# Performance work log

Hardware: AMD Instinct MI355X
Metric: run time of the kernel (lower is better)

## Reference

```python
import jax, jax.numpy as jnp
import numpy as np
from jax import lax

VOCAB = 400000
EMB = 300
HIDDEN = 128
OUT = 3
SEQ = 4096


def setup_inputs() -> dict:
    key = jax.random.key(0)
    ks = jax.random.split(key, 8)
    X = jax.random.randint(ks[0], (SEQ,), 0, VOCAB)
    weights = jax.random.normal(ks[1], (VOCAB, EMB), dtype=jnp.float32) * 0.1
    # nn.RNN params (tanh nonlinearity), uniform(-1/sqrt(H), 1/sqrt(H)) like torch
    s = 1.0 / np.sqrt(HIDDEN)
    W_ih = jax.random.uniform(ks[2], (HIDDEN, EMB), minval=-s, maxval=s, dtype=jnp.float32)
    b_ih = jax.random.uniform(ks[3], (HIDDEN,), minval=-s, maxval=s, dtype=jnp.float32)
    W_hh = jax.random.uniform(ks[4], (HIDDEN, HIDDEN), minval=-s, maxval=s, dtype=jnp.float32)
    b_hh = jax.random.uniform(ks[5], (HIDDEN,), minval=-s, maxval=s, dtype=jnp.float32)
    W_fc = jax.random.uniform(ks[6], (OUT, HIDDEN), minval=-s, maxval=s, dtype=jnp.float32)
    b_fc = jax.random.uniform(ks[7], (OUT,), minval=-s, maxval=s, dtype=jnp.float32)
    return {"X": X, "weights": weights, "W_ih": W_ih, "b_ih": b_ih,
            "W_hh": W_hh, "b_hh": b_hh, "W_fc": W_fc, "b_fc": b_fc}


def reference(X, weights, W_ih, b_ih, W_hh, b_hh, W_fc, b_fc):
    # embedding lookup: [S, E]
    emb = weights[X]
    # precompute input projections for all timesteps in one GEMM: [S, H]
    xproj = emb @ W_ih.T + b_ih
    h0 = jnp.zeros((HIDDEN,), dtype=weights.dtype)

    def step(h, xp):
        h_new = jnp.tanh(xp + h @ W_hh.T + b_hh)
        return h_new, None

    hT, _ = lax.scan(step, h0, xproj)  # Elman recurrence; hT is last-step output
    logits = hT @ W_fc.T + b_fc        # [OUT]; equals fc(yt).squeeze()
    return jax.nn.log_softmax(logits)  # log-softmax over the class dim
```

## Files before the change

kernel.cpp:

```cpp
#include <hip/hip_runtime.h>
#include <hip/hip_bf16.h>

#define VOCAB  400000
#define EMB    300
#define HIDDEN 128
#define OUT    3
#define SEQ    4096
#define SPB    8
#define CHUNK  64
#define NCHUNK (SEQ / CHUNK)

typedef float f32x4 __attribute__((ext_vector_type(4)));

__global__ __launch_bounds__(128) void xproj_kernel(
    const int* __restrict__ X, const float* __restrict__ weights,
    const float* __restrict__ W_ih, const float* __restrict__ b_ih,
    float* __restrict__ xproj)
{
    __shared__ float emb[SPB][EMB];
    __shared__ int xs[SPB];
    const int tid = threadIdx.x;
    const int s0 = blockIdx.x * SPB;

    if (tid < SPB) xs[tid] = X[s0 + tid];
    __syncthreads();

    {
        const float4* w4 = (const float4*)weights;
        float4* e4 = (float4*)&emb[0][0];
        for (int i = tid; i < SPB * (EMB / 4); i += 128) {
            int s = i / (EMB / 4);
            int r = i - s * (EMB / 4);
            e4[i] = w4[(size_t)xs[s] * (EMB / 4) + r];
        }
    }
    __syncthreads();

    const float4* wrow = (const float4*)(W_ih + tid * EMB);
    float acc[SPB];
    #pragma unroll
    for (int s = 0; s < SPB; ++s) acc[s] = 0.f;

    #pragma unroll 5
    for (int r = 0; r < EMB / 4; ++r) {
        float4 w = wrow[r];
        #pragma unroll
        for (int s = 0; s < SPB; ++s) {
            float4 e = *(const float4*)&emb[s][4 * r];
            acc[s] += w.x * e.x;
            acc[s] += w.y * e.y;
            acc[s] += w.z * e.z;
            acc[s] += w.w * e.w;
        }
    }

    const float b = b_ih[tid];
    #pragma unroll
    for (int s = 0; s < SPB; ++s)
        xproj[(size_t)(s0 + s) * HIDDEN + tid] = acc[s] + b;
}

__device__ __forceinline__ float quad_reduce_add(float x) {
    int t = __builtin_amdgcn_update_dpp(0, __float_as_int(x), 0xB1, 0xF, 0xF, true);
    x += __int_as_float(t);
    t = __builtin_amdgcn_update_dpp(0, __float_as_int(x), 0x4E, 0xF, 0xF, true);
    x += __int_as_float(t);
    return x;
}

__global__ __launch_bounds__(512, 2) void rnn_scan_kernel(
    const float* __restrict__ xproj, const float* __restrict__ W_hh,
    const float* __restrict__ b_hh, const float* __restrict__ W_fc,
    const float* __restrict__ b_fc, float* __restrict__ out)
{
    __shared__ float h_lds[2][HIDDEN];
    __shared__ float xp_lds[2][CHUNK * HIDDEN];
    __shared__ float lg[OUT];

    const int tid = threadIdx.x;
    const int o   = tid >> 2;
    const int q   = tid & 3;

    f32x4 w[8];
    {
        const f32x4* wr = (const f32x4*)(W_hh + o * HIDDEN);
        #pragma unroll
        for (int rr = 0; rr < 8; ++rr) w[rr] = wr[4 * rr + q];
        #pragma unroll
        for (int rr = 0; rr < 8; ++rr) asm volatile("" : "+v"(w[rr]));
    }
    const float bh = b_hh[o];

    const f32x4* xp_g4 = (const f32x4*)xproj;
    f32x4 stg[4];
    #pragma unroll
    for (int i = 0; i < 4; ++i) stg[i] = xp_g4[i * 512 + tid];

    if (tid < HIDDEN) h_lds[0][tid] = 0.f;

    int cur = 0;
    for (int t = 0; t < SEQ; ++t) {
        const int tc = t & (CHUNK - 1);
        const int cb = (t >> 6) & 1;
        if (tc == 0) {
            const int c = t >> 6;
            f32x4* dst = (f32x4*)&xp_lds[c & 1][0];
            #pragma unroll
            for (int i = 0; i < 4; ++i) dst[i * 512 + tid] = stg[i];
            __syncthreads();
            const int cn = (c + 1 < NCHUNK) ? c + 1 : NCHUNK - 1;
            #pragma unroll
            for (int i = 0; i < 4; ++i)
                stg[i] = xp_g4[(size_t)cn * (CHUNK * HIDDEN / 4) + i * 512 + tid];
        }

        const float xp = xp_lds[cb][tc * HIDDEN + o];

        const f32x4* hb = (const f32x4*)&h_lds[cur][0] + q;
        float a0 = 0.f, a1 = 0.f, a2 = 0.f, a3 = 0.f;
        #pragma unroll
        for (int rr = 0; rr < 8; ++rr) {
            f32x4 hv = hb[4 * rr];
            a0 += hv[0] * w[rr][0];
            a1 += hv[1] * w[rr][1];
            a2 += hv[2] * w[rr][2];
            a3 += hv[3] * w[rr][3];
        }
        float acc = (a0 + a1) + (a2 + a3);
        acc = quad_reduce_add(acc);

        float z = acc + xp + bh;
        z = fminf(fmaxf(z, -15.f), 15.f);
        float e = __expf(2.f * z);
        float hn = (e - 1.f) * __builtin_amdgcn_rcpf(e + 1.f);
        if (q == 0) h_lds[cur ^ 1][o] = hn;

        __syncthreads();
        cur ^= 1;
    }

    if (tid < OUT) {
        float a = b_fc[tid];
        const float* wf = W_fc + tid * HIDDEN;
        #pragma unroll 4
        for (int j = 0; j < HIDDEN; ++j) a += h_lds[cur][j] * wf[j];
        lg[tid] = a;
    }
    __syncthreads();
    if (tid == 0) {
        float m = fmaxf(lg[0], fmaxf(lg[1], lg[2]));
        float s = expf(lg[0] - m) + expf(lg[1] - m) + expf(lg[2] - m);
        float lse = m + logf(s);
        out[0] = lg[0] - lse;
        out[1] = lg[1] - lse;
        out[2] = lg[2] - lse;
    }
}

extern "C" void kernel_launch(void* const* d_in, const int* in_sizes, int n_in,
                              void* d_out, int out_size, void* d_ws, size_t ws_size,
                              hipStream_t stream) {
    const int*   X       = (const int*)d_in[0];
    const float* weights = (const float*)d_in[1];
    const float* W_ih    = (const float*)d_in[2];
    const float* b_ih    = (const float*)d_in[3];
    const float* W_hh    = (const float*)d_in[4];
    const float* b_hh    = (const float*)d_in[5];
    const float* W_fc    = (const float*)d_in[6];
    const float* b_fc    = (const float*)d_in[7];
    float* out   = (float*)d_out;
    float* xproj = (float*)d_ws;

    xproj_kernel<<<SEQ / SPB, 128, 0, stream>>>(X, weights, W_ih, b_ih, xproj);
    rnn_scan_kernel<<<1, 512, 0, stream>>>(xproj, W_hh, b_hh, W_fc, b_fc, out);
}
```

Baseline: 1.964 ms.

## Remap RNN scan to 16-lane rows computing four outputs with swizzled h

The recurrent matvec now gives each group of 16 lanes four hidden outputs. Each lane holds a slice of 8 columns for each of those four rows and reads only two float4 of h, where it previously read eight. Partial sums are reduced across the 16 lanes with row_shr DPP steps. The h buffer is stored with a padded swizzle to avoid LDS bank conflicts. The per-step __syncthreads is replaced by an explicit lgkmcnt wait plus s_barrier. The intent is to cut LDS traffic and latency on the serial 4096-step critical path, at the cost of more DPP reduction steps and select logic per step.

```diff
diff --git a/kernel.cpp b/kernel.cpp
--- a/kernel.cpp
+++ b/kernel.cpp
@@ -11,6 +11,8 @@
 #define NCHUNK (SEQ / CHUNK)
 
 typedef float f32x4 __attribute__((ext_vector_type(4)));
+
+#define SWZ(s) ((s) + ((s) >> 3))
 
 __global__ __launch_bounds__(128) void xproj_kernel(
     const int* __restrict__ X, const float* __restrict__ weights,
@@ -60,12 +62,22 @@
         xproj[(size_t)(s0 + s) * HIDDEN + tid] = acc[s] + b;
 }
 
-__device__ __forceinline__ float quad_reduce_add(float x) {
-    int t = __builtin_amdgcn_update_dpp(0, __float_as_int(x), 0xB1, 0xF, 0xF, true);
-    x += __int_as_float(t);
-    t = __builtin_amdgcn_update_dpp(0, __float_as_int(x), 0x4E, 0xF, 0xF, true);
-    x += __int_as_float(t);
+template <int CTRL>
+__device__ __forceinline__ float dpp_add(float x) {
+    int t = __builtin_amdgcn_update_dpp(0, __float_as_int(x), CTRL, 0xF, 0xF, true);
+    return x + __int_as_float(t);
+}
+__device__ __forceinline__ float row16_reduce_add(float x) {
+    x = dpp_add<0x128>(x);
+    x = dpp_add<0x124>(x);
+    x = dpp_add<0x4E>(x);
+    x = dpp_add<0xB1>(x);
     return x;
+}
+
+__device__ __forceinline__ void step_barrier() {
+    asm volatile("s_waitcnt lgkmcnt(0)" ::: "memory");
+    __builtin_amdgcn_s_barrier();
 }
 
 __global__ __launch_bounds__(512, 2) void rnn_scan_kernel(
@@ -73,77 +85,88 @@
     const float* __restrict__ b_hh, const float* __restrict__ W_fc,
     const float* __restrict__ b_fc, float* __restrict__ out)
 {
-    __shared__ float h_lds[2][HIDDEN];
+    __shared__ f32x4 h_swz[2][36];
     __shared__ float xp_lds[2][CHUNK * HIDDEN];
     __shared__ float lg[OUT];
 
-    const int tid = threadIdx.x;
-    const int o   = tid >> 2;
-    const int q   = tid & 3;
+    const int tid   = threadIdx.x;
+    const int li    = tid & 15;
+    const int og    = tid >> 4;
+    const int obase = og * 4;
 
-    f32x4 w[8];
-    {
-        const f32x4* wr = (const f32x4*)(W_hh + o * HIDDEN);
+    f32x4 wv[4][2];
+    #pragma unroll
+    for (int oo = 0; oo < 4; ++oo)
         #pragma unroll
-        for (int rr = 0; rr < 8; ++rr) w[rr] = wr[4 * rr + q];
-        #pragma unroll
-        for (int rr = 0; rr < 8; ++rr) asm volatile("" : "+v"(w[rr]));
-    }
-    const float bh = b_hh[o];
+        for (int j = 0; j < 2; ++j)
+            wv[oo][j] = *(const f32x4*)(W_hh + (obase + oo) * HIDDEN + 8 * li + 4 * j);
+    #pragma unroll
+    for (int oo = 0; oo < 4; ++oo)
+        asm volatile("" : "+v"(wv[oo][0]), "+v"(wv[oo][1]));
+
+    const float bh = b_hh[obase + (li & 3)];
 
     const f32x4* xp_g4 = (const f32x4*)xproj;
     f32x4 stg[4];
     #pragma unroll
     for (int i = 0; i < 4; ++i) stg[i] = xp_g4[i * 512 + tid];
 
-    if (tid < HIDDEN) h_lds[0][tid] = 0.f;
+    if (tid < 72) ((f32x4*)h_swz)[tid] = (f32x4)0.f;
+
+    const int rd_slot = SWZ(2 * li);
+    const int wr_dw   = 4 * SWZ(og) + (li & 3);
 
     int cur = 0;
     for (int t = 0; t < SEQ; ++t) {
         const int tc = t & (CHUNK - 1);
-        const int cb = (t >> 6) & 1;
         if (tc == 0) {
             const int c = t >> 6;
             f32x4* dst = (f32x4*)&xp_lds[c & 1][0];
             #pragma unroll
             for (int i = 0; i < 4; ++i) dst[i * 512 + tid] = stg[i];
-            __syncthreads();
+            step_barrier();
             const int cn = (c + 1 < NCHUNK) ? c + 1 : NCHUNK - 1;
             #pragma unroll
             for (int i = 0; i < 4; ++i)
                 stg[i] = xp_g4[(size_t)cn * (CHUNK * HIDDEN / 4) + i * 512 + tid];
         }
 
-        const float xp = xp_lds[cb][tc * HIDDEN + o];
+        const f32x4 hv0 = h_swz[cur][rd_slot];
+        const f32x4 hv1 = h_swz[cur][rd_slot + 1];
 
-        const f32x4* hb = (const f32x4*)&h_lds[cur][0] + q;
-        float a0 = 0.f, a1 = 0.f, a2 = 0.f, a3 = 0.f;
+        float p[4];
         #pragma unroll
-        for (int rr = 0; rr < 8; ++rr) {
-            f32x4 hv = hb[4 * rr];
-            a0 += hv[0] * w[rr][0];
-            a1 += hv[1] * w[rr][1];
-            a2 += hv[2] * w[rr][2];
-            a3 += hv[3] * w[rr][3];
+        for (int oo = 0; oo < 4; ++oo) {
+            f32x4 a = hv0 * wv[oo][0] + hv1 * wv[oo][1];
+            p[oo] = (a[0] + a[1]) + (a[2] + a[3]);
         }
-        float acc = (a0 + a1) + (a2 + a3);
-        acc = quad_reduce_add(acc);
+        #pragma unroll
+        for (int oo = 0; oo < 4; ++oo) p[oo] = row16_reduce_add(p[oo]);
 
-        float z = acc + xp + bh;
+        float v = p[0];
+        v = ((li & 3) == 1) ? p[1] : v;
+        v = ((li & 3) == 2) ? p[2] : v;
+        v = ((li & 3) == 3) ? p[3] : v;
+
+        const float xp = xp_lds[(t >> 6) & 1][tc * HIDDEN + obase + (li & 3)];
+        float z = v + xp + bh;
         z = fminf(fmaxf(z, -15.f), 15.f);
-        float e = __expf(2.f * z);
-        float hn = (e - 1.f) * __builtin_amdgcn_rcpf(e + 1.f);
-        if (q == 0) h_lds[cur ^ 1][o] = hn;
+        float e2 = __expf(2.f * z);
+        float hn = (e2 - 1.f) * __builtin_amdgcn_rcpf(e2 + 1.f);
+        if (li < 4) ((float*)&h_swz[cur ^ 1][0])[wr_dw] = hn;
 
-        __syncthreads();
+        step_barrier();
         cur ^= 1;
     }
 
     if (tid < OUT) {
         float a = b_fc[tid];
+        const float* hp = (const float*)&h_swz[cur][0];
         const float* wf = W_fc + tid * HIDDEN;
-        #pragma unroll 4
-        for (int j = 0; j < HIDDEN; ++j) a += h_lds[cur][j] * wf[j];
+        for (int j = 0; j < HIDDEN; ++j) {
+            int s4 = j >> 2;
+            a += hp[4 * SWZ(s4) + (j & 3)] * wf[j];
+        }
         lg[tid] = a;
     }
     __syncthreads();
```

New measurement: 2.309 ms. 1.18x slower.
